# Performance work log

Measured on AMD Instinct MI355X. Metric: run time of the kernel, lower is better.

Reference implementation:

```python
import jax, jax.numpy as jnp
import numpy as np

KS = 10       # kernel_size
OUT_N = 10    # pred_frames_num
DCT_N = 10
BN_INV = 1.0 / np.sqrt(1.0 + 1e-5)  # BN eval with running_mean=0, running_var=1


def _get_dct_matrix(N):
    k = np.arange(N)[:, None].astype(np.float64)
    i = np.arange(N)[None, :].astype(np.float64)
    w = np.full((N, 1), np.sqrt(2.0 / N))
    w[0, 0] = np.sqrt(1.0 / N)
    dct_m = w * np.cos(np.pi * (i + 0.5) * k / N)
    idct_m = np.linalg.inv(dct_m)
    return dct_m.astype(np.float32), idct_m.astype(np.float32)


def _conv1d(x, w):
    # x: [B, Cin, L], w: [Cout, Cin, K] -> [B, Cout, L-K+1]
    return jax.lax.conv_general_dilated(x, w, (1,), 'VALID',
                                        dimension_numbers=('NCH', 'OIH', 'NCH'))


def setup_inputs() -> dict:
    keys = iter(jax.random.split(jax.random.key(0), 32))
    def rn(shape, s=0.06):
        return (jax.random.normal(next(keys), shape, jnp.float32) * s)
    d = {}
    d['src'] = jax.random.normal(next(keys), (128, 50, 66), jnp.float32)
    d['convQ_w1'] = rn((256, 66, 6)); d['convQ_w2'] = rn((256, 256, 5))
    d['convK_w1'] = rn((256, 66, 6)); d['convK_w2'] = rn((256, 256, 5))
    d['gc1_w'] = rn((20, 256)); d['gc1_att'] = rn((66, 66)); d['gc1_b'] = rn((256,))
    d['bn1_g'] = 1.0 + rn((16896,), 0.1); d['bn1_b'] = rn((16896,), 0.1)
    d['gcb_w1'] = rn((12, 256, 256)); d['gcb_att1'] = rn((12, 66, 66)); d['gcb_b1'] = rn((12, 256))
    d['gcb_bn1_g'] = 1.0 + rn((12, 16896), 0.1); d['gcb_bn1_b'] = rn((12, 16896), 0.1)
    d['gcb_w2'] = rn((12, 256, 256)); d['gcb_att2'] = rn((12, 66, 66)); d['gcb_b2'] = rn((12, 256))
    d['gcb_bn2_g'] = 1.0 + rn((12, 16896), 0.1); d['gcb_bn2_b'] = rn((12, 16896), 0.1)
    d['gc7_w'] = rn((256, 20)); d['gc7_att'] = rn((66, 66)); d['gc7_b'] = rn((20,))
    return d


def reference(src, convQ_w1, convQ_w2, convK_w1, convK_w2,
              gc1_w, gc1_att, gc1_b, bn1_g, bn1_b,
              gcb_w1, gcb_att1, gcb_b1, gcb_bn1_g, gcb_bn1_b,
              gcb_w2, gcb_att2, gcb_b2, gcb_bn2_g, gcb_bn2_b,
              gc7_w, gc7_att, gc7_b):
    bs, input_n, F = src.shape  # [128, 50, 66]
    dct_np, idct_np = _get_dct_matrix(KS + OUT_N)
    dct_m = jnp.asarray(dct_np)
    idct_m = jnp.asarray(idct_np)

    src_t = jnp.transpose(src, (0, 2, 1))             # [bs, F, T]
    src_key = src_t[:, :, :input_n - OUT_N]           # [bs, F, 40]
    src_query = src_t[:, :, -KS:]                     # [bs, F, 10]

    vn = input_n - KS - OUT_N + 1                     # 31
    vl = KS + OUT_N                                   # 20
    idx = np.arange(vl)[None, :] + np.arange(vn)[:, None]   # [vn, vl]
    src_value = src[:, idx].reshape(bs * vn, vl, F)   # sliding windows
    src_value = jnp.matmul(dct_m[:DCT_N], src_value)  # [bs*vn, 10, F]
    src_value = src_value.reshape(bs, vn, DCT_N, F).transpose(0, 1, 3, 2).reshape(bs, vn, F * DCT_N)

    key = jax.nn.relu(_conv1d(jax.nn.relu(_conv1d(src_key / 1000.0, convK_w1)), convK_w2))    # [bs,256,31]
    query = jax.nn.relu(_conv1d(jax.nn.relu(_conv1d(src_query / 1000.0, convQ_w1)), convQ_w2))  # [bs,256,1]

    score = jnp.matmul(query.transpose(0, 2, 1), key) + 1e-15   # [bs,1,31]
    att = score / jnp.sum(score, axis=2, keepdims=True)
    dct_att = jnp.matmul(att, src_value)[:, 0].reshape(bs, F, DCT_N)  # [bs,66,10]

    idx2 = np.concatenate([np.arange(input_n - KS, input_n), np.full(OUT_N, input_n - 1)])
    input_gcn = src[:, idx2]                                   # [bs,20,66]
    dct_in = jnp.matmul(dct_m[:DCT_N], input_gcn).transpose(0, 2, 1)  # [bs,66,10]
    x = jnp.concatenate([dct_in, dct_att], axis=-1)            # [bs,66,20]

    def gconv(h, A, W, b):
        # support = h @ W ; out = A @ support + b
        return jnp.einsum('nm,bmf->bnf', A, h @ W) + b

    def bn(h, g, b):
        sh = h.shape
        return (h.reshape(sh[0], -1) * (g * BN_INV) + b).reshape(sh)

    y = jnp.tanh(bn(gconv(x, gc1_att, gc1_w, gc1_b), bn1_g, bn1_b))  # [bs,66,256]

    def block(y, p):
        w1, a1, b1, g1, be1, w2, a2, b2, g2, be2 = p
        h = jnp.tanh(bn(gconv(y, a1, w1, b1), g1, be1))
        h = jnp.tanh(bn(gconv(h, a2, w2, b2), g2, be2))
        return h + y, None

    y, _ = jax.lax.scan(block, y, (gcb_w1, gcb_att1, gcb_b1, gcb_bn1_g, gcb_bn1_b,
                                   gcb_w2, gcb_att2, gcb_b2, gcb_bn2_g, gcb_bn2_b))

    y = gconv(y, gc7_att, gc7_w, gc7_b) + x                    # [bs,66,20]
    out_gcn = jnp.matmul(idct_m[:, :DCT_N], y[:, :, :DCT_N].transpose(0, 2, 1))  # [bs,20,66]
    return out_gcn[:, :, None, :]                              # [bs,20,1,66] (itera=1)
```

## Files before the change

### kernel.cpp

```cpp
#include <hip/hip_runtime.h>
#include <hip/hip_bf16.h>


typedef __attribute__((ext_vector_type(8))) short short8;
typedef __attribute__((ext_vector_type(4))) float float4v;
typedef __attribute__((ext_vector_type(4))) unsigned uint4v;

#define BNI 0.9999950000374995f

__device__ __forceinline__ short f2bf(float x){
  unsigned u = __float_as_uint(x);
  unsigned r = (u + 0x7fff + ((u >> 16) & 1)) >> 16;
  return (short)r;
}
__device__ __forceinline__ unsigned pk2(float a, float b){
  return (unsigned)(unsigned short)f2bf(a) | ((unsigned)(unsigned short)f2bf(b) << 16);
}
__device__ __forceinline__ float tanh_f(float x){
  x = fminf(fmaxf(x, -9.f), 9.f);
  float e = __expf(2.f * x);
  return (e - 1.f) * __builtin_amdgcn_rcpf(e + 1.f);
}

__global__ __launch_bounds__(256) void k_prep(
    const float* __restrict__ wK1, const float* __restrict__ wQ1,
    const float* __restrict__ wK2, const float* __restrict__ wQ2,
    const float* __restrict__ gw1, const float* __restrict__ gw2,
    const float* __restrict__ gc1_w,
    const float* __restrict__ g0, const float* __restrict__ be0, const float* __restrict__ b0,
    const float* __restrict__ g1a, const float* __restrict__ be1a, const float* __restrict__ b1a,
    const float* __restrict__ g2a, const float* __restrict__ be2a, const float* __restrict__ b2a,
    float* __restrict__ dct, short* __restrict__ w1T, short* __restrict__ w2T,
    short* __restrict__ wgT, short* __restrict__ gc1wT, unsigned* __restrict__ bnP)
{
  __shared__ short tle[64][72];
  int bid = blockIdx.x, tid = threadIdx.x;
  if (bid < 2){
    int t = bid*256 + tid;
    if (t < 400){
      int k = t / 20, i = t % 20;
      double w = (k == 0) ? sqrt(1.0/20.0) : sqrt(2.0/20.0);
      dct[t] = (float)(w * cos(3.14159265358979323846 * (i + 0.5) * k / 20.0));
    }
  } else if (bid < 1026){
    int idx = (bid-2)*256 + tid;
    int f = idx >> 9, k = idx & 511;
    float v = 0.f;
    if (k < 396){
      int h = k / 66, c = k - h*66;
      const float* s = (f < 256) ? wK1 : wQ1;
      v = s[((f & 255)*66 + c)*6 + h];
    }
    w1T[idx] = f2bf(v);
  } else if (bid < 3586){
    int idx = (bid-1026)*256 + tid;
    int f = idx / 1280, k = idx - f*1280;
    int h = k >> 8, c = k & 255;
    const float* s = (f < 256) ? wK2 : wQ2;
    w2T[idx] = f2bf(s[((f & 255)*256 + c)*5 + h]);
  } else if (bid < 3970){
    int q = bid - 3586;
    int l = q >> 4, sub = q & 15;
    int kt = (sub >> 2)*64, ft = (sub & 3)*64;
    const float* s = (l < 12) ? (gw1 + l*65536) : (gw2 + (l-12)*65536);
    int c = tid & 63, r4 = tid >> 6;
    #pragma unroll
    for (int p = 0; p < 16; p++){
      int k = p*4 + r4;
      tle[k][c] = f2bf(s[(kt + k)*256 + ft + c]);
    }
    __syncthreads();
    #pragma unroll
    for (int p = 0; p < 16; p++){
      int f = p*4 + r4;
      wgT[l*65536 + (ft + f)*256 + kt + c] = tle[c][f];
    }
  } else if (bid < 4002){
    int idx = (bid-3970)*256 + tid;
    int f = idx >> 5, k = idx & 31;
    gc1wT[idx] = f2bf(k < 20 ? gc1_w[k*256 + f] : 0.f);
  } else {
    int idx = (bid-4002)*256 + tid;
    if (idx < 25*16896){
      int li = idx / 16896, r = idx - li*16896;
      int f = r & 255;
      const float *g, *be, *bi;
      if (li == 0){ g = g0; be = be0; bi = b0; }
      else {
        int l = (li - 1) >> 1;
        if (li & 1){ g = g1a + l*16896; be = be1a + l*16896; bi = b1a + l*256; }
        else       { g = g2a + l*16896; be = be2a + l*16896; bi = b2a + l*256; }
      }
      float sc = g[r] * BNI;
      float sh = bi[f] * sc + be[r];
      bnP[idx] = pk2(sc, sh);
    }
  }
}

__global__ __launch_bounds__(256) void k_conv1(const float* __restrict__ src,
    const short* __restrict__ w1T, short* __restrict__ kc1q){
  int b = blockIdx.x, ns = blockIdx.y;
  int f0 = ns*128;
  __shared__ short Aim[48*424];
  __shared__ short Wt[128*72];
  int tid = threadIdx.x;
  for (int idx = tid; idx < 48*424; idx += 256){
    int t = idx / 424, kk = idx - t*424;
    float v = 0.f;
    if (kk < 396 && t < 40){
      int h = kk / 66, c = kk - h*66;
      int row = t + h + ((t >= 35) ? 5 : 0);
      v = src[(b*50 + row)*66 + c] * 1e-3f;
    }
    Aim[idx] = f2bf(v);
  }
  int w = tid >> 6, lane = tid & 63, fl = lane & 15, g = lane >> 4;
  float4v acc[3][2];
  #pragma unroll
  for (int i=0;i<3;i++) for (int n=0;n<2;n++) acc[i][n] = (float4v){0.f,0.f,0.f,0.f};
  for (int kt = 0; kt < 416; kt += 64){
    __syncthreads();
    for (int ch = tid; ch < 128*8; ch += 256){
      int r = ch >> 3, kq = ch & 7;
      *(short8*)&Wt[r*72 + kq*8] = *(const short8*)&w1T[(f0 + r)*512 + kt + kq*8];
    }
    __syncthreads();
    int nst = (416 - kt >= 64) ? 2 : 1;
    for (int s = 0; s < nst; s++){
      int k0 = s*32;
      short8 bfr0 = *(const short8*)&Wt[(w*32 + fl)*72 + k0 + g*8];
      short8 bfr1 = *(const short8*)&Wt[(w*32 + 16 + fl)*72 + k0 + g*8];
      #pragma unroll
      for (int i=0;i<3;i++){
        short8 afr = *(const short8*)&Aim[(i*16 + fl)*424 + kt + k0 + g*8];
        acc[i][0] = __builtin_amdgcn_mfma_f32_16x16x32_bf16(afr, bfr0, acc[i][0], 0,0,0);
        acc[i][1] = __builtin_amdgcn_mfma_f32_16x16x32_bf16(afr, bfr1, acc[i][1], 0,0,0);
      }
    }
  }
  #pragma unroll
  for (int i=0;i<3;i++) for (int n=0;n<2;n++) for (int j=0;j<4;j++){
    int t = i*16 + g*4 + j;
    int f = f0 + w*32 + n*16 + fl;
    float v = fmaxf(acc[i][n][j], 0.f);
    if (t < 35 && f < 256) kc1q[(b*40 + t)*256 + f] = f2bf(v);
    else if (t >= 35 && t < 40 && f >= 256) kc1q[(b*40 + t)*256 + (f - 256)] = f2bf(v);
  }
}

__global__ __launch_bounds__(256) void k_conv2(const short* __restrict__ kc1q,
    const short* __restrict__ w2T, float* __restrict__ key, float* __restrict__ q){
  int b = blockIdx.x, ns = blockIdx.y;
  int f0 = ns*128;
  __shared__ short kcs[40*256];
  __shared__ short Wt[128*136];
  char* kcb = (char*)kcs;
  int tid = threadIdx.x;
  for (int ch = tid; ch < 1280; ch += 256){
    int r = ch >> 5, kq = ch & 31;
    unsigned byte = (unsigned)(r*512 + kq*16) ^ (unsigned)((r & 7) << 4);
    *(short8*)(kcb + byte) = *(const short8*)&kc1q[(b*40 + r)*256 + kq*8];
  }
  int w = tid >> 6, lane = tid & 63, fl = lane & 15, g = lane >> 4;
  float4v acc[2][2];
  #pragma unroll
  for (int i=0;i<2;i++) for (int n=0;n<2;n++) acc[i][n] = (float4v){0.f,0.f,0.f,0.f};
  for (int kt = 0; kt < 1280; kt += 128){
    __syncthreads();
    for (int ch = tid; ch < 128*16; ch += 256){
      int r = ch >> 4, kq = ch & 15;
      *(short8*)&Wt[r*136 + kq*8] = *(const short8*)&w2T[(f0 + r)*1280 + kt + kq*8];
    }
    __syncthreads();
    #pragma unroll
    for (int s = 0; s < 4; s++){
      int k = kt + s*32;
      int h = k >> 8, cb = k & 255;
      short8 bfr0 = *(const short8*)&Wt[(w*32 + fl)*136 + s*32 + g*8];
      short8 bfr1 = *(const short8*)&Wt[(w*32 + 16 + fl)*136 + s*32 + g*8];
      #pragma unroll
      for (int i=0;i<2;i++){
        int t = i*16 + fl;
        int row = t + h + ((t == 31) ? 4 : 0);
        unsigned byte = (unsigned)(row*512 + (cb + g*8)*2) ^ (unsigned)((row & 7) << 4);
        short8 afr = *(const short8*)(kcb + byte);
        acc[i][0] = __builtin_amdgcn_mfma_f32_16x16x32_bf16(afr, bfr0, acc[i][0], 0,0,0);
        acc[i][1] = __builtin_amdgcn_mfma_f32_16x16x32_bf16(afr, bfr1, acc[i][1], 0,0,0);
      }
    }
  }
  #pragma unroll
  for (int i=0;i<2;i++) for (int n=0;n<2;n++) for (int j=0;j<4;j++){
    int t = i*16 + g*4 + j;
    int f = f0 + w*32 + n*16 + fl;
    float v = fmaxf(acc[i][n][j], 0.f);
    if (t < 31 && f < 256) key[(b*31 + t)*256 + f] = v;
    else if (t == 31 && f >= 256) q[b*256 + f - 256] = v;
  }
}

__global__ __launch_bounds__(64) void k_att(const float* __restrict__ q,
    const float* __restrict__ key, float* __restrict__ att){
  int b = blockIdx.x;
  int lane = threadIdx.x;
  float s = 0.f;
  if (lane < 31){
    const float* kr = key + (b*31 + lane)*256;
    const float* qr = q + b*256;
    for (int o = 0; o < 256; o++) s += qr[o] * kr[o];
    s += 1e-15f;
  }
  float tot = s;
  for (int off = 32; off; off >>= 1) tot += __shfl_down(tot, off);
  tot = __shfl(tot, 0);
  if (lane < 31) att[b*32 + lane] = s / tot;
}

__global__ __launch_bounds__(256) void k_build_x(const float* __restrict__ src,
    const float* __restrict__ att, const float* __restrict__ dct,
    float* __restrict__ x, short* __restrict__ x_bf){
  int b = blockIdx.x;
  int tid = threadIdx.x;
  __shared__ float z[20*66];
  __shared__ float a[31];
  for (int i = tid; i < 2560; i += 256) x_bf[b*2560 + i] = 0;
  if (tid < 31) a[tid] = att[b*32 + tid];
  __syncthreads();
  for (int idx = tid; idx < 1320; idx += 256){
    int i = idx / 66, f = idx % 66;
    float s = 0.f;
    for (int v = 0; v < 31; v++) s += a[v] * src[(b*50 + v + i)*66 + f];
    z[idx] = s;
  }
  __syncthreads();
  for (int idx = tid; idx < 660; idx += 256){
    int f = idx / 10, k = idx % 10;
    float s1 = 0.f, s2 = 0.f;
    #pragma unroll
    for (int i = 0; i < 20; i++){
      float d = dct[k*20 + i];
      int tt = (i < 10) ? (40 + i) : 49;
      s1 += d * src[(b*50 + tt)*66 + f];
      s2 += d * z[i*66 + f];
    }
    x[(b*66 + f)*20 + k] = s1;
    x[(b*66 + f)*20 + 10 + k] = s2;
    x_bf[(b*80 + f)*32 + k] = f2bf(s1);
    x_bf[(b*80 + f)*32 + 10 + k] = f2bf(s2);
  }
}


__device__ __forceinline__ void am_addr(int i, const float* __restrict__ Af,
    uint2* u, int* byt){
  int n = i / 24, mq = (i % 24) * 4;
  float v0=0.f, v1=0.f, v2=0.f, v3=0.f;
  if (n < 66){
    if (mq+0 < 66) v0 = Af[n*66 + mq+0];
    if (mq+1 < 66) v1 = Af[n*66 + mq+1];
    if (mq+2 < 66) v2 = Af[n*66 + mq+2];
    if (mq+3 < 66) v3 = Af[n*66 + mq+3];
  }
  u->x = pk2(v0, v1); u->y = pk2(v2, v3);
  *byt = n*256 + ((mq*2) ^ ((n & 15) << 4));
}

__device__ __forceinline__ void stage_Am(const float* __restrict__ Af, int tid,
    char* am_c){
  for (int i = tid; i < 1920; i += 512){
    uint2 u; int byt;
    am_addr(i, Af, &u, &byt);
    *(uint2*)(am_c + byt) = u;
  }
}

template<int KSTEPS, int KSTRIDE, int MODE>
__device__ __forceinline__ void layer_step(
    const short* __restrict__ Wg,
    const unsigned* __restrict__ bnl, const float* __restrict__ Af,
    float4v (&y_r)[2][5], int tid, int w, int fl, int g,
    char* __restrict__ ybf_c, char* __restrict__ tT_c, char* __restrict__ am_c)
{
  const short* wbase = Wg + (w*32 + fl)*KSTRIDE + g*8;
  short8 bw[3][2];
  bw[0][0] = *(const short8*)(wbase);
  bw[0][1] = *(const short8*)(wbase + 16*KSTRIDE);
  if (KSTEPS > 1){
    bw[1][0] = *(const short8*)(wbase + 32);
    bw[1][1] = *(const short8*)(wbase + 16*KSTRIDE + 32);
  }
  uint2 amu[4]; int amb[4];
  #pragma unroll
  for (int s=0;s<4;s++){
    int i = tid + s*512;
    if (i < 1920) am_addr(i, Af, &amu[s], &amb[s]); else amb[s] = -1;
  }

  float4v acc[5][2];
  #pragma unroll
  for (int i=0;i<5;i++){ acc[i][0]=(float4v){0.f,0.f,0.f,0.f}; acc[i][1]=(float4v){0.f,0.f,0.f,0.f}; }
  #pragma unroll
  for (int ks=0; ks<KSTEPS; ks++){
    if (ks + 2 < KSTEPS){
      bw[(ks+2)%3][0] = *(const short8*)(wbase + (ks+2)*32);
      bw[(ks+2)%3][1] = *(const short8*)(wbase + 16*KSTRIDE + (ks+2)*32);
    }
    #pragma unroll
    for (int i=0;i<5;i++){
      int m = i*16 + fl;
      short8 af = *(const short8*)(ybf_c + m*512 + ((ks*64 + g*16) ^ ((m & 15) << 4)));
      acc[i][0] = __builtin_amdgcn_mfma_f32_16x16x32_bf16(af, bw[ks%3][0], acc[i][0], 0,0,0);
      acc[i][1] = __builtin_amdgcn_mfma_f32_16x16x32_bf16(af, bw[ks%3][1], acc[i][1], 0,0,0);
    }
  }
  #pragma unroll
  for (int i=0;i<5;i++){
    int mb = (i*16 + g*4)*2;
    #pragma unroll
    for (int n=0;n<2;n++){
      int f = w*32 + n*16 + fl;
      uint2 u; u.x = pk2(acc[i][n][0], acc[i][n][1]); u.y = pk2(acc[i][n][2], acc[i][n][3]);
      *(uint2*)(tT_c + f*256 + (mb ^ ((f & 15) << 4))) = u;
    }
  }
  #pragma unroll
  for (int s=0;s<4;s++) if (amb[s] >= 0) *(uint2*)(am_c + amb[s]) = amu[s];
  __syncthreads();

  uint4v bnp0[5], bnp1[5];
  #pragma unroll
  for (int n2=0;n2<5;n2++){
    int n = n2*16 + fl; int ns = (n < 66) ? n : 0;
    bnp0[n2] = *(const uint4v*)&bnl[ns*256 + w*32 + g*4];
  }
  float4v a2[2][5];
  #pragma unroll
  for (int i=0;i<2;i++)
    #pragma unroll
    for (int n=0;n<5;n++) a2[i][n] = (float4v){0.f,0.f,0.f,0.f};

#define G2STEP(ks) { \
    short8 bA[5]; \
    _Pragma("unroll") \
    for (int n2=0;n2<5;n2++){ \
      int n = n2*16 + fl; \
      bA[n2] = *(const short8*)(am_c + n*256 + (((ks)*64 + g*16) ^ ((n & 15) << 4))); \
    } \
    _Pragma("unroll") \
    for (int i2=0;i2<2;i2++){ \
      int f = w*32 + i2*16 + fl; \
      short8 af = *(const short8*)(tT_c + f*256 + (((ks)*64 + g*16) ^ ((f & 15) << 4))); \
      _Pragma("unroll") \
      for (int n2=0;n2<5;n2++) \
        a2[i2][n2] = __builtin_amdgcn_mfma_f32_16x16x32_bf16(af, bA[n2], a2[i2][n2], 0,0,0); \
    } }

  G2STEP(0)
  #pragma unroll
  for (int n2=0;n2<5;n2++){
    int n = n2*16 + fl; int ns = (n < 66) ? n : 0;
    bnp1[n2] = *(const uint4v*)&bnl[ns*256 + w*32 + 16 + g*4];
  }
  G2STEP(1)
  G2STEP(2)
#undef G2STEP

  #pragma unroll
  for (int i2=0;i2<2;i2++){
    #pragma unroll
    for (int n2=0;n2<5;n2++){
      int n = n2*16 + fl;
      bool nok = (n < 66);
      float vv[4];
      #pragma unroll
      for (int j=0;j<4;j++){
        unsigned u = (i2 == 0) ? bnp0[n2][j] : bnp1[n2][j];
        float sc = __uint_as_float((u & 0xffffu) << 16);
        float sh = __uint_as_float(u & 0xffff0000u);
        float v = a2[i2][n2][j]*sc + sh;
        v = tanh_f(v);
        if (MODE == 0) y_r[i2][n2][j] = v;
        if (MODE == 2){ v += y_r[i2][n2][j]; y_r[i2][n2][j] = v; }
        vv[j] = nok ? v : 0.f;
      }
      int fb2 = (w*32 + i2*16 + g*4)*2;
      uint2 u2; u2.x = pk2(vv[0], vv[1]); u2.y = pk2(vv[2], vv[3]);
      *(uint2*)(ybf_c + n*512 + (fb2 ^ ((n & 15) << 4))) = u2;
    }
  }
  __syncthreads();
}

__global__ __launch_bounds__(512) void k_mega(const short* __restrict__ x_bf,
    const short* __restrict__ gc1wT, const short* __restrict__ wgT,
    const float* __restrict__ gc1_att,
    const float* __restrict__ a1, const float* __restrict__ a2m,
    const unsigned* __restrict__ bnP,
    const float* __restrict__ gc7_w, const float* __restrict__ gc7_att,
    const float* __restrict__ gc7_b, const float* __restrict__ x,
    const float* __restrict__ dct, float* __restrict__ out)
{
  __shared__ __align__(16) char ybf_c[40960];
  __shared__ __align__(16) char tT_c[65536];
  __shared__ __align__(16) char am_c[20480];
  __shared__ float xo_l[1320];
  __shared__ float dct_l[400];

  int b = blockIdx.x, tid = threadIdx.x;
  int w = tid >> 6, lane = tid & 63, fl = lane & 15, g = lane >> 4;

  for (int i = tid; i < 4096; i += 512) ((float4v*)tT_c)[i] = (float4v){0.f,0.f,0.f,0.f};
  for (int i = tid; i < 400; i += 512) dct_l[i] = dct[i];
  for (int i = tid; i < 320; i += 512){
    int m = i >> 2, kq = i & 3;
    short8 v = *(const short8*)&x_bf[(b*80 + m)*32 + kq*8];
    *(short8*)(ybf_c + m*512 + ((kq*16) ^ ((m & 15) << 4))) = v;
  }
  __syncthreads();

  float4v y_r[2][5];

  layer_step<1,32,0>(gc1wT, bnP, gc1_att, y_r, tid, w, fl, g, ybf_c, tT_c, am_c);
  for (int l = 0; l < 12; l++){
    layer_step<8,256,1>(wgT + l*65536, bnP + (1+2*l)*16896, a1 + l*4356,
                        y_r, tid, w, fl, g, ybf_c, tT_c, am_c);
    layer_step<8,256,2>(wgT + (12+l)*65536, bnP + (2+2*l)*16896, a2m + l*4356,
                        y_r, tid, w, fl, g, ybf_c, tT_c, am_c);
  }

  for (int i = tid; i < 2048; i += 512){
    int f = i >> 6, kq = (i & 63)*4;
    float v0=0.f, v1=0.f, v2=0.f, v3=0.f;
    if (f < 20){
      v0 = gc7_w[(kq+0)*20 + f]; v1 = gc7_w[(kq+1)*20 + f];
      v2 = gc7_w[(kq+2)*20 + f]; v3 = gc7_w[(kq+3)*20 + f];
    }
    uint2 u; u.x = pk2(v0, v1); u.y = pk2(v2, v3);
    *(uint2*)(am_c + f*512 + ((kq*2) ^ ((f & 15) << 4))) = u;
  }
  __syncthreads();

  float4v at[5][2];
  #pragma unroll
  for (int i=0;i<5;i++){ at[i][0] = (float4v){0.f,0.f,0.f,0.f}; at[i][1] = (float4v){0.f,0.f,0.f,0.f}; }
  #pragma unroll
  for (int ks = 0; ks < 8; ks++){
    short8 bf[2];
    #pragma unroll
    for (int n=0;n<2;n++){
      int f = n*16 + fl;
      bf[n] = *(const short8*)(am_c + f*512 + ((ks*64 + g*16) ^ ((f & 15) << 4)));
    }
    #pragma unroll
    for (int i=0;i<5;i++){
      int m = i*16 + fl;
      short8 af = *(const short8*)(ybf_c + m*512 + ((ks*64 + g*16) ^ ((m & 15) << 4)));
      at[i][0] = __builtin_amdgcn_mfma_f32_16x16x32_bf16(af, bf[0], at[i][0], 0,0,0);
      at[i][1] = __builtin_amdgcn_mfma_f32_16x16x32_bf16(af, bf[1], at[i][1], 0,0,0);
    }
  }
  if (w == 0){
    #pragma unroll
    for (int i=0;i<5;i++){
      int mb = (i*16 + g*4)*2;
      #pragma unroll
      for (int n=0;n<2;n++){
        int f = n*16 + fl;
        uint2 u; u.x = pk2(at[i][n][0], at[i][n][1]); u.y = pk2(at[i][n][2], at[i][n][3]);
        *(uint2*)(tT_c + f*256 + (mb ^ ((f & 15) << 4))) = u;
      }
    }
  }
  __syncthreads();
  stage_Am(gc7_att, tid, am_c);
  __syncthreads();

  float4v a2t[2][5];
  #pragma unroll
  for (int i=0;i<2;i++)
    #pragma unroll
    for (int n=0;n<5;n++) a2t[i][n] = (float4v){0.f,0.f,0.f,0.f};
  #pragma unroll
  for (int ks = 0; ks < 3; ks++){
    short8 bA[5];
    #pragma unroll
    for (int n2=0;n2<5;n2++){
      int n = n2*16 + fl;
      bA[n2] = *(const short8*)(am_c + n*256 + ((ks*64 + g*16) ^ ((n & 15) << 4)));
    }
    #pragma unroll
    for (int i2=0;i2<2;i2++){
      int f = i2*16 + fl;
      short8 af = *(const short8*)(tT_c + f*256 + ((ks*64 + g*16) ^ ((f & 15) << 4)));
      #pragma unroll
      for (int n2=0;n2<5;n2++)
        a2t[i2][n2] = __builtin_amdgcn_mfma_f32_16x16x32_bf16(af, bA[n2], a2t[i2][n2], 0,0,0);
    }
  }
  if (w == 0){
    #pragma unroll
    for (int i2=0;i2<2;i2++){
      #pragma unroll
      for (int n2=0;n2<5;n2++){
        int n = n2*16 + fl;
        #pragma unroll
        for (int j=0;j<4;j++){
          int f = i2*16 + g*4 + j;
          if (f < 20 && n < 66)
            xo_l[n*20 + f] = a2t[i2][n2][j] + gc7_b[f] + x[(b*66 + n)*20 + f];
        }
      }
    }
  }
  __syncthreads();

  for (int idx = tid; idx < 1320; idx += 512){
    int r = idx / 66, fn = idx % 66;
    float s = 0.f;
    #pragma unroll
    for (int k = 0; k < 10; k++) s += dct_l[k*20 + r] * xo_l[fn*20 + k];
    out[(b*20 + r)*66 + fn] = s;
  }
}

extern "C" void kernel_launch(void* const* d_in, const int* in_sizes, int n_in,
                              void* d_out, int out_size, void* d_ws, size_t ws_size,
                              hipStream_t stream) {
  const float* src      = (const float*)d_in[0];
  const float* convQ_w1 = (const float*)d_in[1];
  const float* convQ_w2 = (const float*)d_in[2];
  const float* convK_w1 = (const float*)d_in[3];
  const float* convK_w2 = (const float*)d_in[4];
  const float* gc1_w    = (const float*)d_in[5];
  const float* gc1_att  = (const float*)d_in[6];
  const float* gc1_b    = (const float*)d_in[7];
  const float* bn1_g    = (const float*)d_in[8];
  const float* bn1_b    = (const float*)d_in[9];
  const float* gcb_w1   = (const float*)d_in[10];
  const float* gcb_att1 = (const float*)d_in[11];
  const float* gcb_b1   = (const float*)d_in[12];
  const float* gcb_bn1g = (const float*)d_in[13];
  const float* gcb_bn1b = (const float*)d_in[14];
  const float* gcb_w2   = (const float*)d_in[15];
  const float* gcb_att2 = (const float*)d_in[16];
  const float* gcb_b2   = (const float*)d_in[17];
  const float* gcb_bn2g = (const float*)d_in[18];
  const float* gcb_bn2b = (const float*)d_in[19];
  const float* gc7_w    = (const float*)d_in[20];
  const float* gc7_att  = (const float*)d_in[21];
  const float* gc7_b    = (const float*)d_in[22];
  float* out = (float*)d_out;

  float* ws    = (float*)d_ws;
  float* dct   = ws;
  float* x     = ws + 512;
  short* x_bf  = (short*)(ws + 169472);
  short* wgT   = (short*)(ws + 333312);
  short* gc1wT = (short*)(ws + 1119744);
  short* w1T   = (short*)(ws + 1123840);
  short* w2T   = (short*)(ws + 1254912);
  short* kc1q  = (short*)(ws + 1582592);
  float* key   = ws + 2237952;
  float* q     = ws + 3253760;
  float* att   = ws + 3286528;
  unsigned* bnP= (unsigned*)(ws + 3290624);

  k_prep<<<5652, 256, 0, stream>>>(convK_w1, convQ_w1, convK_w2, convQ_w2,
      gcb_w1, gcb_w2, gc1_w,
      bn1_g, bn1_b, gc1_b, gcb_bn1g, gcb_bn1b, gcb_b1,
      gcb_bn2g, gcb_bn2b, gcb_b2,
      dct, w1T, w2T, wgT, gc1wT, bnP);

  k_conv1<<<dim3(128,4), 256, 0, stream>>>(src, w1T, kc1q);
  k_conv2<<<dim3(128,4), 256, 0, stream>>>(kc1q, w2T, key, q);
  k_att<<<128, 64, 0, stream>>>(q, key, att);
  k_build_x<<<128, 256, 0, stream>>>(src, att, dct, x, x_bf);

  k_mega<<<128, 512, 0, stream>>>(x_bf, gc1wT, wgT, gc1_att,
      gcb_att1, gcb_att2, bnP,
      gc7_w, gc7_att, gc7_b, x, dct, out);
}
```

Baseline: 304.2 us.

## Fuse attention into build_x, use hardware bf16 pack, raise MFMA priority

Merges the attention-score kernel into the x-building kernel and splits each dot product across 8 threads with a shared-memory reduction, removing one launch and the att round trip. Replaces the software bf16 rounding in pk2 with the v_cvt_pk_bf16_f32 instruction. Wraps the MFMA loops in s_setprio to favour matrix issue, and rewrites some LDS offset expressions in an equivalent form. The hardware conversion must round the same way as the software version.

```diff
diff --git a/kernel.cpp b/kernel.cpp
--- a/kernel.cpp
+++ b/kernel.cpp
@@ -14,7 +14,9 @@
   return (short)r;
 }
 __device__ __forceinline__ unsigned pk2(float a, float b){
-  return (unsigned)(unsigned short)f2bf(a) | ((unsigned)(unsigned short)f2bf(b) << 16);
+  unsigned r;
+  asm("v_cvt_pk_bf16_f32 %0, %1, %2" : "=v"(r) : "v"(a), "v"(b));
+  return r;
 }
 __device__ __forceinline__ float tanh_f(float x){
   x = fminf(fmaxf(x, -9.f), 9.f);
@@ -200,32 +202,39 @@
   }
 }
 
-__global__ __launch_bounds__(64) void k_att(const float* __restrict__ q,
-    const float* __restrict__ key, float* __restrict__ att){
-  int b = blockIdx.x;
-  int lane = threadIdx.x;
-  float s = 0.f;
-  if (lane < 31){
-    const float* kr = key + (b*31 + lane)*256;
-    const float* qr = q + b*256;
-    for (int o = 0; o < 256; o++) s += qr[o] * kr[o];
-    s += 1e-15f;
-  }
-  float tot = s;
-  for (int off = 32; off; off >>= 1) tot += __shfl_down(tot, off);
-  tot = __shfl(tot, 0);
-  if (lane < 31) att[b*32 + lane] = s / tot;
-}
-
-__global__ __launch_bounds__(256) void k_build_x(const float* __restrict__ src,
-    const float* __restrict__ att, const float* __restrict__ dct,
-    float* __restrict__ x, short* __restrict__ x_bf){
+__global__ __launch_bounds__(256) void k_attx(const float* __restrict__ src,
+    const float* __restrict__ q, const float* __restrict__ key,
+    const float* __restrict__ dct, float* __restrict__ x, short* __restrict__ x_bf){
   int b = blockIdx.x;
   int tid = threadIdx.x;
+  __shared__ float sred[31][9];
+  __shared__ float a[31];
   __shared__ float z[20*66];
-  __shared__ float a[31];
   for (int i = tid; i < 2560; i += 256) x_bf[b*2560 + i] = 0;
-  if (tid < 31) a[tid] = att[b*32 + tid];
+  if (tid < 248){
+    int v = tid >> 3, p = tid & 7;
+    const float* kr = key + (b*31 + v)*256 + p*32;
+    const float* qr = q + b*256 + p*32;
+    float s = 0.f;
+    #pragma unroll
+    for (int o = 0; o < 32; o++) s += qr[o] * kr[o];
+    sred[v][p] = s;
+  }
+  __syncthreads();
+  if (tid < 31){
+    float s = 1e-15f;
+    #pragma unroll
+    for (int p = 0; p < 8; p++) s += sred[tid][p];
+    sred[tid][8] = s;
+  }
+  __syncthreads();
+  if (tid < 64){
+    float v = (tid < 31) ? sred[tid][8] : 0.f;
+    float tot = v;
+    for (int off = 32; off; off >>= 1) tot += __shfl_down(tot, off);
+    tot = __shfl(tot, 0);
+    if (tid < 31) a[tid] = v / tot;
+  }
   __syncthreads();
   for (int idx = tid; idx < 1320; idx += 256){
     int i = idx / 66, f = idx % 66;
@@ -300,6 +309,7 @@
   float4v acc[5][2];
   #pragma unroll
   for (int i=0;i<5;i++){ acc[i][0]=(float4v){0.f,0.f,0.f,0.f}; acc[i][1]=(float4v){0.f,0.f,0.f,0.f}; }
+  __builtin_amdgcn_s_setprio(1);
   #pragma unroll
   for (int ks=0; ks<KSTEPS; ks++){
     if (ks + 2 < KSTEPS){
@@ -314,6 +324,7 @@
       acc[i][1] = __builtin_amdgcn_mfma_f32_16x16x32_bf16(af, bw[ks%3][1], acc[i][1], 0,0,0);
     }
   }
+  __builtin_amdgcn_s_setprio(0);
   #pragma unroll
   for (int i=0;i<5;i++){
     int mb = (i*16 + g*4)*2;
@@ -356,6 +367,7 @@
         a2[i2][n2] = __builtin_amdgcn_mfma_f32_16x16x32_bf16(af, bA[n2], a2[i2][n2], 0,0,0); \
     } }
 
+  __builtin_amdgcn_s_setprio(1);
   G2STEP(0)
   #pragma unroll
   for (int n2=0;n2<5;n2++){
@@ -364,6 +376,7 @@
   }
   G2STEP(1)
   G2STEP(2)
+  __builtin_amdgcn_s_setprio(0);
 #undef G2STEP
 
   #pragma unroll
@@ -450,12 +463,12 @@
     #pragma unroll
     for (int n=0;n<2;n++){
       int f = n*16 + fl;
-      bf[n] = *(const short8*)(am_c + f*512 + ((ks*64 + g*16) ^ ((f & 15) << 4)));
+      bf[n] = *(const short8*)(am_c + f*512 + (((ks*32 + g*8)*2) ^ ((f & 15) << 4)));
     }
     #pragma unroll
     for (int i=0;i<5;i++){
       int m = i*16 + fl;
-      short8 af = *(const short8*)(ybf_c + m*512 + ((ks*64 + g*16) ^ ((m & 15) << 4)));
+      short8 af = *(const short8*)(ybf_c + m*512 + (((ks*32 + g*8)*2) ^ ((m & 15) << 4)));
       at[i][0] = __builtin_amdgcn_mfma_f32_16x16x32_bf16(af, bf[0], at[i][0], 0,0,0);
       at[i][1] = __builtin_amdgcn_mfma_f32_16x16x32_bf16(af, bf[1], at[i][1], 0,0,0);
     }
@@ -487,12 +500,12 @@
     #pragma unroll
     for (int n2=0;n2<5;n2++){
       int n = n2*16 + fl;
-      bA[n2] = *(const short8*)(am_c + n*256 + ((ks*64 + g*16) ^ ((n & 15) << 4)));
+      bA[n2] = *(const short8*)(am_c + n*256 + (((ks*32 + g*8)*2) ^ ((n & 15) << 4)));
     }
     #pragma unroll
     for (int i2=0;i2<2;i2++){
       int f = i2*16 + fl;
-      short8 af = *(const short8*)(tT_c + f*256 + ((ks*64 + g*16) ^ ((f & 15) << 4)));
+      short8 af = *(const short8*)(tT_c + f*256 + (((ks*32 + g*8)*2) ^ ((f & 15) << 4)));
       #pragma unroll
       for (int n2=0;n2<5;n2++)
         a2t[i2][n2] = __builtin_amdgcn_mfma_f32_16x16x32_bf16(af, bA[n2], a2t[i2][n2], 0,0,0);
@@ -563,7 +576,6 @@
   short* kc1q  = (short*)(ws + 1582592);
   float* key   = ws + 2237952;
   float* q     = ws + 3253760;
-  float* att   = ws + 3286528;
   unsigned* bnP= (unsigned*)(ws + 3290624);
 
   k_prep<<<5652, 256, 0, stream>>>(convK_w1, convQ_w1, convK_w2, convQ_w2,
@@ -574,8 +586,7 @@
 
   k_conv1<<<dim3(128,4), 256, 0, stream>>>(src, w1T, kc1q);
   k_conv2<<<dim3(128,4), 256, 0, stream>>>(kc1q, w2T, key, q);
-  k_att<<<128, 64, 0, stream>>>(q, key, att);
-  k_build_x<<<128, 256, 0, stream>>>(src, att, dct, x, x_bf);
+  k_attx<<<128, 256, 0, stream>>>(src, q, key, dct, x, x_bf);
 
   k_mega<<<128, 512, 0, stream>>>(x_bf, gc1wT, wgT, gc1_att,
       gcb_att1, gcb_att2, bnP,
```

Result: faster. 290.6 us (-4.5%).
